# Optimization experiments

Hardware: AMD Instinct MI355X
Metric: run time of the kernel (lower is better)

## Reference

```python
import jax, jax.numpy as jnp
import numpy as np

INPUT_DIM = 16
LW = 128          # layerwidth
NB_LAYERS = 4
NB_X = 4096
NB_THETA = 128
PARAM_COUNT = INPUT_DIM * LW + LW + (NB_LAYERS - 1) * (LW * LW + LW) + LW + 1  # 51841


def setup_inputs() -> dict:
    k1, k2 = jax.random.split(jax.random.key(0))
    x = jax.random.normal(k1, (NB_X, INPUT_DIM), dtype=jnp.float32)
    theta = jax.random.normal(k2, (NB_THETA, PARAM_COUNT), dtype=jnp.float32)
    return {"x": x, "theta": theta}


def reference(x, theta):
    # x: [nb_x, input_dim], theta: [nb_theta, param_count]
    t = theta.shape[0]
    off = 0
    # first layer: W0 [t, LW, INPUT_DIM], b0 [t, LW]
    W0 = theta[:, off:off + INPUT_DIM * LW].reshape(t, LW, INPUT_DIM); off += INPUT_DIM * LW
    b0 = theta[:, off:off + LW]; off += LW
    h = jnp.tanh(jnp.einsum('thi,xi->txh', W0, x) + b0[:, None, :])  # [t, nb_x, LW]
    # hidden layers
    for _ in range(NB_LAYERS - 1):
        W = theta[:, off:off + LW * LW].reshape(t, LW, LW); off += LW * LW
        b = theta[:, off:off + LW]; off += LW
        h = jnp.tanh(jnp.einsum('tho,txo->txh', W, h) + b[:, None, :])
    # output layer: Wl [t, LW], bl [t, 1]
    Wl = theta[:, off:off + LW]; off += LW
    bl = theta[:, off:off + 1]
    out = jnp.einsum('th,txh->tx', Wl, h)[..., None] + bl[:, None, :]  # [t, nb_x, 1]
    return out
```

## Files before the change

### kernel.cpp

```cpp
#include <hip/hip_runtime.h>


#define IND      16
#define LWD      128
#define THREADS  256
#define PARAMS   51841

#define HID_STRIDE 36864
#define WS_W0    (128 * 3 * HID_STRIDE)
#define WS_XI    (WS_W0 + 128 * 16384)
#define WS_TOTAL (WS_XI + 32 * 8192)

#define LDS_WL   36864
#define LDS_BL   37376
#define LDS_SZ   37380

typedef _Float16 f16x8 __attribute__((ext_vector_type(8)));
typedef _Float16 f16x4 __attribute__((ext_vector_type(4)));
typedef float    f32x16 __attribute__((ext_vector_type(16)));
typedef unsigned u32x2  __attribute__((ext_vector_type(2)));

union U4 { unsigned u[4]; f16x8 v; };

__device__ __forceinline__ f32x16 zero16() {
    f32x16 z;
#pragma unroll
    for (int i = 0; i < 16; ++i) z[i] = 0.0f;
    return z;
}
__device__ __forceinline__ float fast_tanh(float v) {
    float e = __builtin_amdgcn_exp2f(v * 2.8853900817779268f);
    return 1.0f - 2.0f * __builtin_amdgcn_rcpf(e + 1.0f);
}
__device__ __forceinline__ unsigned pkf16(float a, float b) {
    unsigned short ua = __builtin_bit_cast(unsigned short, (_Float16)a);
    unsigned short ub = __builtin_bit_cast(unsigned short, (_Float16)b);
    return (unsigned)ua | ((unsigned)ub << 16);
}
#define MFMA(A, B, C) __builtin_amdgcn_mfma_f32_32x32x16_f16((A), (B), (C), 0, 0, 0)

__device__ __forceinline__ void gload16(const void* g, void* l) {
    __builtin_amdgcn_global_load_lds(
        (const __attribute__((address_space(1))) void*)g,
        (__attribute__((address_space(3))) void*)l, 16, 0, 0);
}

__device__ __forceinline__ void conv8(const float* __restrict__ s, char* hidst, char* lodst) {
    float v[8];
    *reinterpret_cast<float4*>(v)     = *reinterpret_cast<const float4*>(s);
    *reinterpret_cast<float4*>(v + 4) = *reinterpret_cast<const float4*>(s + 4);
    f16x8 hi, lo;
#pragma unroll
    for (int i = 0; i < 8; ++i) {
        hi[i] = (_Float16)v[i];
        lo[i] = (_Float16)(v[i] - (float)hi[i]);
    }
    *reinterpret_cast<f16x8*>(hidst) = hi;
    *reinterpret_cast<f16x8*>(lodst) = lo;
}

__global__ __launch_bounds__(256)
void prep_kernel(const float* __restrict__ theta, const float* __restrict__ xin,
                 char* __restrict__ ws)
{
    const int b = blockIdx.x, tid = threadIdx.x;
    if (b < 3072) {
        const int t = b / 24, rem = b % 24, li = rem >> 3, hblk = rem & 7;
        const int h  = hblk * 16 + (tid >> 4);
        const int kc = (tid >> 1) & 7, kh = tid & 1;
        const float* src = theta + (size_t)t * PARAMS + 2176 + li * 16512
                         + h * 128 + kc * 16 + kh * 8;
        float v[8];
        *reinterpret_cast<float4*>(v)     = *reinterpret_cast<const float4*>(src);
        *reinterpret_cast<float4*>(v + 4) = *reinterpret_cast<const float4*>(src + 4);
        f16x8 p;
#pragma unroll
        for (int i = 0; i < 8; ++i) p[i] = (_Float16)v[i];
        char* img = ws + (size_t)(t * 3 + li) * HID_STRIDE;
        *reinterpret_cast<f16x8*>(img + ((h >> 5) * 9 + kc) * 1024
                                      + (kh * 32 + (h & 31)) * 16) = p;
    } else if (b < 3456) {
        const int idx = b - 3072, t = idx / 3, li = idx % 3;
        const int tt = tid >> 6, l6 = tid & 63, kh = l6 >> 5, row = l6 & 31;
        f16x8 p;
#pragma unroll
        for (int i = 0; i < 8; ++i) p[i] = (_Float16)0.0f;
        if (kh == 0) {
            const float bv = theta[(size_t)t * PARAMS + 2176 + li * 16512
                                   + 16384 + tt * 32 + row];
            p[0] = (_Float16)bv;
            p[1] = (_Float16)(bv - (float)p[0]);
        }
        char* img = ws + (size_t)(t * 3 + li) * HID_STRIDE;
        *reinterpret_cast<f16x8*>(img + (tt * 9 + 8) * 1024 + l6 * 16) = p;
    } else if (b < 3520) {
        const int gid = (b - 3456) * 256 + tid;
        const int t = gid >> 7, h = gid & 127;
        const float* src = theta + (size_t)t * PARAMS + h * IND;
        char* dst = ws + WS_W0 + (size_t)t * 16384 + h * 32;
        conv8(src,     dst,      dst + 4096);
        conv8(src + 8, dst + 16, dst + 4096 + 16);
    } else if (b < 3648) {
        const int t = b - 3520;
        const float* th = theta + (size_t)t * PARAMS;
        char* base = ws + WS_W0 + (size_t)t * 16384;
        {
            const int tt = tid >> 6, l6 = tid & 63, kh = l6 >> 5, row = l6 & 31;
            f16x8 p;
#pragma unroll
            for (int i = 0; i < 8; ++i) p[i] = (_Float16)0.0f;
            if (kh == 0) {
                const float bv = th[2048 + tt * 32 + row];
                p[0] = (_Float16)bv;
                p[1] = (_Float16)(bv - (float)p[0]);
            }
            *reinterpret_cast<f16x8*>(base + 8192 + tt * 1024 + l6 * 16) = p;
        }
        if (tid < 32) {
            const int kc = tid >> 1, kh = tid & 1;
            const float* src = th + 51712 + kc * 16 + kh * 8;
            f16x8 p;
#pragma unroll
            for (int i = 0; i < 8; ++i) p[i] = (_Float16)src[i];
            *reinterpret_cast<f16x8*>(base + 12288 + tid * 16) = p;
        }
    } else {
        const int row = (b - 3648) * 256 + tid;
        const float* src = xin + (size_t)row * IND;
        char* dst = ws + WS_XI + (size_t)(row >> 7) * 8192 + (row & 127) * 32;
        conv8(src,     dst,      dst + 4096);
        conv8(src + 8, dst + 16, dst + 4096 + 16);
    }
}

__global__ __launch_bounds__(THREADS, 4)
void mlp_main(const float* __restrict__ theta, const char* __restrict__ ws,
              float* __restrict__ out)
{
    __shared__ __align__(16) char sL[LDS_SZ];

    const int tid = threadIdx.x, bid = blockIdx.x;
    const int sw  = (bid & 7) * 512 + (bid >> 3);
    const int t   = sw >> 5, xt = sw & 31;
    const float* __restrict__ th = theta + (size_t)t * PARAMS;
    const int lane = tid & 63, w = tid >> 6, r31 = lane & 31, khalf = lane >> 5;
    const int bpa  = (lane ^ 32) << 2;
    (void)bpa;

    U4 ubias;
    ubias.u[0] = khalf ? 0u : 0x3C003C00u;
    ubias.u[1] = 0u; ubias.u[2] = 0u; ubias.u[3] = 0u;
    const f16x8 Bones = ubias.v;

    {
        const char* img = ws + (size_t)(t * 3) * HID_STRIDE;
#pragma unroll
        for (int c = 0; c < 9; ++c)
            gload16(img + (c * 4 + w) * 1024 + lane * 16, sL + (c * 4 + w) * 1024);
        if (tid < 32)
            gload16(ws + WS_W0 + (size_t)t * 16384 + 12288 + tid * 16,
                    sL + LDS_WL + tid * 16);
        if (tid == 32) *reinterpret_cast<float*>(sL + LDS_BL) = th[51840];
    }

    f32x16 acc[4];
    {
        const char* w0i = ws + WS_W0 + (size_t)t  * 16384;
        const char* xi  = ws + WS_XI + (size_t)xt * 8192;
        const int ro = r31 * 32 + khalf * 16;
        const f16x8 B0h = *reinterpret_cast<const f16x8*>(xi + w * 1024 + ro);
        const f16x8 B0l = *reinterpret_cast<const f16x8*>(xi + 4096 + w * 1024 + ro);
#pragma unroll
        for (int tt = 0; tt < 4; ++tt) {
            f32x16 a = zero16();
            const f16x8 Ab = *reinterpret_cast<const f16x8*>(w0i + 8192 + tt * 1024 + lane * 16);
            a = MFMA(Ab, Bones, a);
            const f16x8 Ah = *reinterpret_cast<const f16x8*>(w0i + tt * 1024 + ro);
            const f16x8 Al = *reinterpret_cast<const f16x8*>(w0i + 4096 + tt * 1024 + ro);
            a = MFMA(Al, B0h, a);
            a = MFMA(Ah, B0l, a);
            a = MFMA(Ah, B0h, a);
            acc[tt] = a;
        }
    }

    f16x8 Bf[8];
    auto activate_pack = [&]() {
#pragma unroll
        for (int tt = 0; tt < 4; ++tt) {
            unsigned P0[4], P1[4];
#pragma unroll
            for (int g = 0; g < 4; ++g) {
                const float v0 = fast_tanh(acc[tt][4 * g + 0]);
                const float v1 = fast_tanh(acc[tt][4 * g + 1]);
                const float v2 = fast_tanh(acc[tt][4 * g + 2]);
                const float v3 = fast_tanh(acc[tt][4 * g + 3]);
                P0[g] = pkf16(v0, v1);
                P1[g] = pkf16(v2, v3);
            }
#pragma unroll
            for (int j = 0; j < 2; ++j) {
#if __has_builtin(__builtin_amdgcn_permlane32_swap)
                const u32x2 r0 = __builtin_amdgcn_permlane32_swap(
                    P0[2 * j], P0[2 * j + 1], false, false);
                const u32x2 r1 = __builtin_amdgcn_permlane32_swap(
                    P1[2 * j], P1[2 * j + 1], false, false);
                U4 u;
                u.u[0] = r0[0]; u.u[1] = r1[0]; u.u[2] = r0[1]; u.u[3] = r1[1];
#else
                const unsigned s0 = khalf ? P0[2 * j] : P0[2 * j + 1];
                const unsigned s1 = khalf ? P1[2 * j] : P1[2 * j + 1];
                const unsigned q0 = (unsigned)__builtin_amdgcn_ds_bpermute(bpa, (int)s0);
                const unsigned q1 = (unsigned)__builtin_amdgcn_ds_bpermute(bpa, (int)s1);
                U4 u;
                u.u[0] = khalf ? q0 : P0[2 * j];
                u.u[1] = khalf ? q1 : P1[2 * j];
                u.u[2] = khalf ? P0[2 * j + 1] : q0;
                u.u[3] = khalf ? P1[2 * j + 1] : q1;
#endif
                Bf[2 * tt + j] = u.v;
            }
        }
    };
    activate_pack();
    __syncthreads();

#pragma unroll
    for (int l = 1; l <= 3; ++l) {
        __builtin_amdgcn_s_setprio(1);
#pragma unroll
        for (int tt = 0; tt < 4; ++tt) {
            f32x16 a = zero16();
            a = MFMA(*reinterpret_cast<const f16x8*>(
                         sL + (tt * 9 + 8) * 1024 + lane * 16), Bones, a);
#pragma unroll
            for (int kc = 0; kc < 8; ++kc) {
                const f16x8 av = *reinterpret_cast<const f16x8*>(
                    sL + (tt * 9 + kc) * 1024 + lane * 16);
                a = MFMA(av, Bf[kc], a);
            }
            acc[tt] = a;
        }
        __builtin_amdgcn_s_setprio(0);
        if (l < 3) {
            __syncthreads();
            const char* img = ws + (size_t)(t * 3 + l) * HID_STRIDE;
#pragma unroll
            for (int c = 0; c < 9; ++c)
                gload16(img + (c * 4 + w) * 1024 + lane * 16, sL + (c * 4 + w) * 1024);
            activate_pack();
            __syncthreads();
        }
    }

    activate_pack();
    const float bl = *reinterpret_cast<const float*>(sL + LDS_BL);
    f32x16 af = zero16();
#pragma unroll
    for (int kc = 0; kc < 8; ++kc) {
        const f16x8 wv = *reinterpret_cast<const f16x8*>(
            sL + LDS_WL + (kc * 2 + khalf) * 16);
        af = MFMA(wv, Bf[kc], af);
    }
    if (!khalf) out[(size_t)t * 4096 + xt * 128 + w * 32 + r31] = af[0] + bl;
}

__global__ __launch_bounds__(THREADS, 1)
void mlp_kernel_fb(const float* __restrict__ xin,
                   const float* __restrict__ theta,
                   float* __restrict__ out)
{
    __shared__ __align__(16) _Float16 sH   [128 * LWD];
    __shared__ __align__(16) _Float16 sWhi [LWD * LWD];
    __shared__ __align__(16) _Float16 sWlo [LWD * LWD];
    __shared__ __align__(16) _Float16 sX0hi[128 * IND];
    __shared__ __align__(16) _Float16 sX0lo[128 * IND];
    __shared__ __align__(16) _Float16 sW0hi[LWD * IND];
    __shared__ __align__(16) _Float16 sW0lo[LWD * IND];
    __shared__ float sB[2][LWD];
    __shared__ float sWl[LWD + 1];

    const int tid = threadIdx.x;
    const int bid = blockIdx.x;
    const int sw  = (bid & 7) * 512 + (bid >> 3);
    const int t   = sw >> 5;
    const int xt  = sw & 31;
    const float* __restrict__ th = theta + (size_t)t * PARAMS;
    const float* __restrict__ xg = xin   + (size_t)xt * (128 * IND);

#pragma unroll
    for (int j = 0; j < 2; ++j) {
        const int flat = j * 1024 + tid * 4;
        const float4 v = *reinterpret_cast<const float4*>(xg + flat);
        _Float16 h0 = (_Float16)v.x, h1 = (_Float16)v.y, h2 = (_Float16)v.z, h3 = (_Float16)v.w;
        f16x4 ph = {h0, h1, h2, h3};
        f16x4 pl = {(_Float16)(v.x - (float)h0), (_Float16)(v.y - (float)h1),
                    (_Float16)(v.z - (float)h2), (_Float16)(v.w - (float)h3)};
        *reinterpret_cast<f16x4*>(&sX0hi[flat]) = ph;
        *reinterpret_cast<f16x4*>(&sX0lo[flat]) = pl;
    }
#pragma unroll
    for (int j = 0; j < 2; ++j) {
        const int flat = j * 1024 + tid * 4;
        const float a0 = th[flat], a1 = th[flat + 1], a2 = th[flat + 2], a3 = th[flat + 3];
        _Float16 h0 = (_Float16)a0, h1 = (_Float16)a1, h2 = (_Float16)a2, h3 = (_Float16)a3;
        f16x4 ph = {h0, h1, h2, h3};
        f16x4 pl = {(_Float16)(a0 - (float)h0), (_Float16)(a1 - (float)h1),
                    (_Float16)(a2 - (float)h2), (_Float16)(a3 - (float)h3)};
        *reinterpret_cast<f16x4*>(&sW0hi[flat]) = ph;
        *reinterpret_cast<f16x4*>(&sW0lo[flat]) = pl;
    }
    if (tid < LWD) sB[0][tid] = th[IND * LWD + tid];
    __syncthreads();

    const int lane  = tid & 63;
    const int w     = tid >> 6;
    const int r31   = lane & 31;
    const int khalf = lane >> 5;
    const int hb    = (w >> 1) * 64;
    const int xb    = (w & 1) * 64;
    const int hA0 = hb + r31,  hA1 = hb + 32 + r31;
    const int xB0 = xb + r31,  xB1 = xb + 32 + r31;
    const int swzA0 = (hA0 & 15) << 4, swzA1 = (hA1 & 15) << 4;
    const int swzB0 = (xB0 & 15) << 4, swzB1 = (xB1 & 15) << 4;

    f32x16 acc[2][2];

    {
        const int kb = khalf * 16;
        f16x8 ah[2], al[2], bh[2], bl[2];
        ah[0] = *reinterpret_cast<const f16x8*>((const char*)sW0hi + hA0 * 32 + kb);
        ah[1] = *reinterpret_cast<const f16x8*>((const char*)sW0hi + hA1 * 32 + kb);
        al[0] = *reinterpret_cast<const f16x8*>((const char*)sW0lo + hA0 * 32 + kb);
        al[1] = *reinterpret_cast<const f16x8*>((const char*)sW0lo + hA1 * 32 + kb);
        bh[0] = *reinterpret_cast<const f16x8*>((const char*)sX0hi + xB0 * 32 + kb);
        bh[1] = *reinterpret_cast<const f16x8*>((const char*)sX0hi + xB1 * 32 + kb);
        bl[0] = *reinterpret_cast<const f16x8*>((const char*)sX0lo + xB0 * 32 + kb);
        bl[1] = *reinterpret_cast<const f16x8*>((const char*)sX0lo + xB1 * 32 + kb);
#pragma unroll
        for (int tt = 0; tt < 2; ++tt)
#pragma unroll
            for (int tx = 0; tx < 2; ++tx) {
                f32x16 a;
#pragma unroll
                for (int i = 0; i < 16; ++i) a[i] = 0.0f;
                a = MFMA(al[tt], bh[tx], a);
                a = MFMA(ah[tt], bl[tx], a);
                a = MFMA(ah[tt], bh[tx], a);
                acc[tt][tx] = a;
            }
    }

    auto epilogue = [&](const float* __restrict__ bb) {
#pragma unroll
        for (int tt = 0; tt < 2; ++tt)
#pragma unroll
            for (int tx = 0; tx < 2; ++tx) {
                const int xw  = xb + tx * 32 + r31;
                const int swz = (xw & 15) << 4;
#pragma unroll
                for (int g = 0; g < 4; ++g) {
                    const int hbase = hb + tt * 32 + g * 8 + khalf * 4;
                    f16x4 pk;
#pragma unroll
                    for (int q = 0; q < 4; ++q) {
                        const float v = acc[tt][tx][g * 4 + q] + bb[hbase + q];
                        pk[q] = (_Float16)(1.0f - 2.0f * __builtin_amdgcn_rcpf(
                            __builtin_amdgcn_exp2f(v * 2.8853900817779268f) + 1.0f));
                    }
                    *reinterpret_cast<f16x4*>((char*)sH + xw * 256 + ((hbase * 2) ^ swz)) = pk;
                }
            }
    };

    for (int l = 0; l < 3; ++l) {
        __syncthreads();
        const float* __restrict__ wsrc = th + 2176 + l * 16512;
#pragma unroll
        for (int j = 0; j < 16; ++j) {
            const int flat = j * 1024 + tid * 4;
            const int hrow = flat >> 7;
            const int o    = flat & 127;
            const float a0 = wsrc[flat], a1 = wsrc[flat + 1], a2 = wsrc[flat + 2], a3 = wsrc[flat + 3];
            _Float16 h0 = (_Float16)a0, h1 = (_Float16)a1, h2 = (_Float16)a2, h3 = (_Float16)a3;
            f16x4 ph = {h0, h1, h2, h3};
            f16x4 pl = {(_Float16)(a0 - (float)h0), (_Float16)(a1 - (float)h1),
                        (_Float16)(a2 - (float)h2), (_Float16)(a3 - (float)h3)};
            const int boff = hrow * 256 + ((o * 2) ^ ((hrow & 15) << 4));
            *reinterpret_cast<f16x4*>((char*)sWhi + boff) = ph;
            *reinterpret_cast<f16x4*>((char*)sWlo + boff) = pl;
        }
        if (tid < LWD) sB[(l + 1) & 1][tid] = wsrc[LWD * LWD + tid];
        if (l == 2) {
            if (tid < LWD) sWl[tid] = th[51712 + tid];
            if (tid == LWD) sWl[LWD] = th[51840];
        }

        epilogue(sB[l & 1]);
        __syncthreads();

#pragma unroll
        for (int tt = 0; tt < 2; ++tt)
#pragma unroll
            for (int tx = 0; tx < 2; ++tx)
#pragma unroll
                for (int i = 0; i < 16; ++i) acc[tt][tx][i] = 0.0f;
#pragma unroll
        for (int kc = 0; kc < 8; ++kc) {
            const int kb = kc * 32 + khalf * 16;
            f16x8 ah[2], al[2], bv[2];
            ah[0] = *reinterpret_cast<const f16x8*>((const char*)sWhi + hA0 * 256 + (kb ^ swzA0));
            ah[1] = *reinterpret_cast<const f16x8*>((const char*)sWhi + hA1 * 256 + (kb ^ swzA1));
            al[0] = *reinterpret_cast<const f16x8*>((const char*)sWlo + hA0 * 256 + (kb ^ swzA0));
            al[1] = *reinterpret_cast<const f16x8*>((const char*)sWlo + hA1 * 256 + (kb ^ swzA1));
            bv[0] = *reinterpret_cast<const f16x8*>((const char*)sH   + xB0 * 256 + (kb ^ swzB0));
            bv[1] = *reinterpret_cast<const f16x8*>((const char*)sH   + xB1 * 256 + (kb ^ swzB1));
#pragma unroll
            for (int tt = 0; tt < 2; ++tt)
#pragma unroll
                for (int tx = 0; tx < 2; ++tx) {
                    acc[tt][tx] = MFMA(al[tt], bv[tx], acc[tt][tx]);
                    acc[tt][tx] = MFMA(ah[tt], bv[tx], acc[tt][tx]);
                }
        }
    }

    __syncthreads();
    epilogue(sB[1]);
    __syncthreads();

    if (tid < 128) {
        const int r   = tid;
        const int swz = (r & 15) << 4;
        float s = 0.0f;
#pragma unroll
        for (int c = 0; c < 16; ++c) {
            const int hc = (c + r) & 15;
            const f16x8 hv = *reinterpret_cast<const f16x8*>(
                (const char*)sH + r * 256 + ((hc * 16) ^ swz));
#pragma unroll
            for (int q = 0; q < 8; ++q) s += (float)hv[q] * sWl[hc * 8 + q];
        }
        out[(size_t)t * 4096 + (size_t)xt * 128 + r] = s + sWl[LWD];
    }
}

extern "C" void kernel_launch(void* const* d_in, const int* in_sizes, int n_in,
                              void* d_out, int out_size, void* d_ws, size_t ws_size,
                              hipStream_t stream)
{
    const float* x     = (const float*)d_in[0];
    const float* theta = (const float*)d_in[1];
    float* out = (float*)d_out;

    if (ws_size >= (size_t)WS_TOTAL) {
        prep_kernel<<<dim3(3664), dim3(256), 0, stream>>>(theta, x, (char*)d_ws);
        mlp_main<<<dim3(4096), dim3(THREADS), 0, stream>>>(theta, (const char*)d_ws, out);
    } else {
        mlp_kernel_fb<<<dim3(4096), dim3(THREADS), 0, stream>>>(x, theta, out);
    }
}
```

Baseline: 109.6 us.

## Interleave tanh packing with MFMA chunks and fold tanh scale into weights

Restructures each hidden layer so the tanh-and-pack of one output tile is interleaved with the MFMA k-chunks that consume already-packed tiles, using double-buffered accumulators. This lets VALU transcendental work overlap the matrix pipeline instead of running as a separate phase. It also pre-multiplies weights and biases by 2/ln2 in the prep kernel, so the activation skips one multiply. The activation itself becomes a sign-symmetric form with a polynomial-plus-Newton reciprocal and a packed round-toward-zero convert. The occupancy hint drops from 4 to 2 blocks per CU, which allows more registers but may cut latency hiding. The weight scaling and the different reciprocal and rounding slightly change numerics.

Measured after the change: 118.4 us. +8.0%, slower.

```diff
diff --git a/kernel.cpp b/kernel.cpp
--- a/kernel.cpp
+++ b/kernel.cpp
@@ -5,6 +5,7 @@
 #define LWD      128
 #define THREADS  256
 #define PARAMS   51841
+#define SCALE    2.8853900817779268f
 
 #define HID_STRIDE 36864
 #define WS_W0    (128 * 3 * HID_STRIDE)
@@ -28,15 +29,22 @@
     for (int i = 0; i < 16; ++i) z[i] = 0.0f;
     return z;
 }
-__device__ __forceinline__ float fast_tanh(float v) {
-    float e = __builtin_amdgcn_exp2f(v * 2.8853900817779268f);
-    return 1.0f - 2.0f * __builtin_amdgcn_rcpf(e + 1.0f);
-}
-__device__ __forceinline__ unsigned pkf16(float a, float b) {
-    unsigned short ua = __builtin_bit_cast(unsigned short, (_Float16)a);
-    unsigned short ub = __builtin_bit_cast(unsigned short, (_Float16)b);
-    return (unsigned)ua | ((unsigned)ub << 16);
-}
+
+__device__ __forceinline__ unsigned tanh2pk(float z0, float z1) {
+    const float t0 = __builtin_amdgcn_exp2f(-__builtin_fabsf(z0));
+    const float t1 = __builtin_amdgcn_exp2f(-__builtin_fabsf(z1));
+    const float d0 = t0 + 1.0f, d1 = t1 + 1.0f;
+    float r0 = __builtin_fmaf(d0, __builtin_fmaf(d0, 0.32302f, -1.45380f), 2.12094f);
+    float r1 = __builtin_fmaf(d1, __builtin_fmaf(d1, 0.32302f, -1.45380f), 2.12094f);
+    r0 = __builtin_fmaf(r0, __builtin_fmaf(-d0, r0, 1.0f), r0);
+    r1 = __builtin_fmaf(r1, __builtin_fmaf(-d1, r1, 1.0f), r1);
+    const float u0 = __builtin_fmaf(t0 * r0, -2.0f, 1.0f);
+    const float u1 = __builtin_fmaf(t1 * r1, -2.0f, 1.0f);
+    const float y0 = __builtin_copysignf(u0, z0);
+    const float y1 = __builtin_copysignf(u1, z1);
+    return __builtin_bit_cast(unsigned, __builtin_amdgcn_cvt_pkrtz(y0, y1));
+}
+
 #define MFMA(A, B, C) __builtin_amdgcn_mfma_f32_32x32x16_f16((A), (B), (C), 0, 0, 0)
 
 __device__ __forceinline__ void gload16(const void* g, void* l) {
@@ -45,15 +53,17 @@
         (__attribute__((address_space(3))) void*)l, 16, 0, 0);
 }
 
-__device__ __forceinline__ void conv8(const float* __restrict__ s, char* hidst, char* lodst) {
+__device__ __forceinline__ void conv8(const float* __restrict__ s, char* hidst,
+                                      char* lodst, float scale) {
     float v[8];
     *reinterpret_cast<float4*>(v)     = *reinterpret_cast<const float4*>(s);
     *reinterpret_cast<float4*>(v + 4) = *reinterpret_cast<const float4*>(s + 4);
     f16x8 hi, lo;
 #pragma unroll
     for (int i = 0; i < 8; ++i) {
-        hi[i] = (_Float16)v[i];
-        lo[i] = (_Float16)(v[i] - (float)hi[i]);
+        const float sv = v[i] * scale;
+        hi[i] = (_Float16)sv;
+        lo[i] = (_Float16)(sv - (float)hi[i]);
     }
     *reinterpret_cast<f16x8*>(hidst) = hi;
     *reinterpret_cast<f16x8*>(lodst) = lo;
@@ -75,7 +85,7 @@
         *reinterpret_cast<float4*>(v + 4) = *reinterpret_cast<const float4*>(src + 4);
         f16x8 p;
 #pragma unroll
-        for (int i = 0; i < 8; ++i) p[i] = (_Float16)v[i];
+        for (int i = 0; i < 8; ++i) p[i] = (_Float16)(v[i] * SCALE);
         char* img = ws + (size_t)(t * 3 + li) * HID_STRIDE;
         *reinterpret_cast<f16x8*>(img + ((h >> 5) * 9 + kc) * 1024
                                       + (kh * 32 + (h & 31)) * 16) = p;
@@ -86,8 +96,8 @@
 #pragma unroll
         for (int i = 0; i < 8; ++i) p[i] = (_Float16)0.0f;
         if (kh == 0) {
-            const float bv = theta[(size_t)t * PARAMS + 2176 + li * 16512
-                                   + 16384 + tt * 32 + row];
+            const float bv = SCALE * theta[(size_t)t * PARAMS + 2176 + li * 16512
+                                           + 16384 + tt * 32 + row];
             p[0] = (_Float16)bv;
             p[1] = (_Float16)(bv - (float)p[0]);
         }
@@ -98,8 +108,8 @@
         const int t = gid >> 7, h = gid & 127;
         const float* src = theta + (size_t)t * PARAMS + h * IND;
         char* dst = ws + WS_W0 + (size_t)t * 16384 + h * 32;
-        conv8(src,     dst,      dst + 4096);
-        conv8(src + 8, dst + 16, dst + 4096 + 16);
+        conv8(src,     dst,      dst + 4096,      SCALE);
+        conv8(src + 8, dst + 16, dst + 4096 + 16, SCALE);
     } else if (b < 3648) {
         const int t = b - 3520;
         const float* th = theta + (size_t)t * PARAMS;
@@ -110,7 +120,7 @@
 #pragma unroll
             for (int i = 0; i < 8; ++i) p[i] = (_Float16)0.0f;
             if (kh == 0) {
-                const float bv = th[2048 + tt * 32 + row];
+                const float bv = SCALE * th[2048 + tt * 32 + row];
                 p[0] = (_Float16)bv;
                 p[1] = (_Float16)(bv - (float)p[0]);
             }
@@ -128,12 +138,12 @@
         const int row = (b - 3648) * 256 + tid;
         const float* src = xin + (size_t)row * IND;
         char* dst = ws + WS_XI + (size_t)(row >> 7) * 8192 + (row & 127) * 32;
-        conv8(src,     dst,      dst + 4096);
-        conv8(src + 8, dst + 16, dst + 4096 + 16);
-    }
-}
-
-__global__ __launch_bounds__(THREADS, 4)
+        conv8(src,     dst,      dst + 4096,      1.0f);
+        conv8(src + 8, dst + 16, dst + 4096 + 16, 1.0f);
+    }
+}
+
+__global__ __launch_bounds__(THREADS, 2)
 void mlp_main(const float* __restrict__ theta, const char* __restrict__ ws,
               float* __restrict__ out)
 {
@@ -151,19 +161,24 @@
     ubias.u[0] = khalf ? 0u : 0x3C003C00u;
     ubias.u[1] = 0u; ubias.u[2] = 0u; ubias.u[3] = 0u;
     const f16x8 Bones = ubias.v;
-
-    {
-        const char* img = ws + (size_t)(t * 3) * HID_STRIDE;
+    const f32x16 Z = zero16();
+
+    auto stage = [&](int l) {
+        const char* img = ws + (size_t)(t * 3 + l) * HID_STRIDE;
 #pragma unroll
         for (int c = 0; c < 9; ++c)
             gload16(img + (c * 4 + w) * 1024 + lane * 16, sL + (c * 4 + w) * 1024);
-        if (tid < 32)
-            gload16(ws + WS_W0 + (size_t)t * 16384 + 12288 + tid * 16,
-                    sL + LDS_WL + tid * 16);
-        if (tid == 32) *reinterpret_cast<float*>(sL + LDS_BL) = th[51840];
-    }
-
-    f32x16 acc[4];
+    };
+
+    stage(0);
+    if (tid < 32)
+        gload16(ws + WS_W0 + (size_t)t * 16384 + 12288 + tid * 16,
+                sL + LDS_WL + tid * 16);
+    if (tid == 32) *reinterpret_cast<float*>(sL + LDS_BL) = th[51840];
+
+    f32x16 accA[4], accB[4];
+    f16x8  Bf[8];
+
     {
         const char* w0i = ws + WS_W0 + (size_t)t  * 16384;
         const char* xi  = ws + WS_XI + (size_t)xt * 8192;
@@ -172,96 +187,99 @@
         const f16x8 B0l = *reinterpret_cast<const f16x8*>(xi + 4096 + w * 1024 + ro);
 #pragma unroll
         for (int tt = 0; tt < 4; ++tt) {
-            f32x16 a = zero16();
             const f16x8 Ab = *reinterpret_cast<const f16x8*>(w0i + 8192 + tt * 1024 + lane * 16);
-            a = MFMA(Ab, Bones, a);
+            f32x16 a = MFMA(Ab, Bones, Z);
             const f16x8 Ah = *reinterpret_cast<const f16x8*>(w0i + tt * 1024 + ro);
             const f16x8 Al = *reinterpret_cast<const f16x8*>(w0i + 4096 + tt * 1024 + ro);
             a = MFMA(Al, B0h, a);
             a = MFMA(Ah, B0l, a);
             a = MFMA(Ah, B0h, a);
-            acc[tt] = a;
-        }
-    }
-
-    f16x8 Bf[8];
-    auto activate_pack = [&]() {
+            accA[tt] = a;
+        }
+    }
+
+    auto pack_tile = [&](const f32x16& a, int bi) {
+        unsigned P0[4], P1[4];
+#pragma unroll
+        for (int g = 0; g < 4; ++g) {
+            P0[g] = tanh2pk(a[4 * g + 0], a[4 * g + 1]);
+            P1[g] = tanh2pk(a[4 * g + 2], a[4 * g + 3]);
+        }
+#pragma unroll
+        for (int j = 0; j < 2; ++j) {
+#if __has_builtin(__builtin_amdgcn_permlane32_swap)
+            const u32x2 r0 = __builtin_amdgcn_permlane32_swap(
+                P0[2 * j], P0[2 * j + 1], false, false);
+            const u32x2 r1 = __builtin_amdgcn_permlane32_swap(
+                P1[2 * j], P1[2 * j + 1], false, false);
+            U4 u;
+            u.u[0] = r0[0]; u.u[1] = r1[0]; u.u[2] = r0[1]; u.u[3] = r1[1];
+#else
+            const unsigned s0 = khalf ? P0[2 * j] : P0[2 * j + 1];
+            const unsigned s1 = khalf ? P1[2 * j] : P1[2 * j + 1];
+            const unsigned q0 = (unsigned)__builtin_amdgcn_ds_bpermute(bpa, (int)s0);
+            const unsigned q1 = (unsigned)__builtin_amdgcn_ds_bpermute(bpa, (int)s1);
+            U4 u;
+            u.u[0] = khalf ? q0 : P0[2 * j];
+            u.u[1] = khalf ? q1 : P1[2 * j];
+            u.u[2] = khalf ? P0[2 * j + 1] : q0;
+            u.u[3] = khalf ? P1[2 * j + 1] : q1;
+#endif
+            Bf[bi + j] = u.v;
+        }
+    };
+
+    auto kchunk = [&](f32x16* aN, int kc) {
 #pragma unroll
         for (int tt = 0; tt < 4; ++tt) {
-            unsigned P0[4], P1[4];
-#pragma unroll
-            for (int g = 0; g < 4; ++g) {
-                const float v0 = fast_tanh(acc[tt][4 * g + 0]);
-                const float v1 = fast_tanh(acc[tt][4 * g + 1]);
-                const float v2 = fast_tanh(acc[tt][4 * g + 2]);
-                const float v3 = fast_tanh(acc[tt][4 * g + 3]);
-                P0[g] = pkf16(v0, v1);
-                P1[g] = pkf16(v2, v3);
-            }
-#pragma unroll
-            for (int j = 0; j < 2; ++j) {
-#if __has_builtin(__builtin_amdgcn_permlane32_swap)
-                const u32x2 r0 = __builtin_amdgcn_permlane32_swap(
-                    P0[2 * j], P0[2 * j + 1], false, false);
-                const u32x2 r1 = __builtin_amdgcn_permlane32_swap(
-                    P1[2 * j], P1[2 * j + 1], false, false);
-                U4 u;
-                u.u[0] = r0[0]; u.u[1] = r1[0]; u.u[2] = r0[1]; u.u[3] = r1[1];
-#else
-                const unsigned s0 = khalf ? P0[2 * j] : P0[2 * j + 1];
-                const unsigned s1 = khalf ? P1[2 * j] : P1[2 * j + 1];
-                const unsigned q0 = (unsigned)__builtin_amdgcn_ds_bpermute(bpa, (int)s0);
-                const unsigned q1 = (unsigned)__builtin_amdgcn_ds_bpermute(bpa, (int)s1);
-                U4 u;
-                u.u[0] = khalf ? q0 : P0[2 * j];
-                u.u[1] = khalf ? q1 : P1[2 * j];
-                u.u[2] = khalf ? P0[2 * j + 1] : q0;
-                u.u[3] = khalf ? P1[2 * j + 1] : q1;
-#endif
-                Bf[2 * tt + j] = u.v;
-            }
+            const f16x8 av = *reinterpret_cast<const f16x8*>(
+                sL + (tt * 9 + kc) * 1024 + lane * 16);
+            aN[tt] = MFMA(av, Bf[kc], aN[tt]);
         }
     };
-    activate_pack();
-    __syncthreads();
-
-#pragma unroll
-    for (int l = 1; l <= 3; ++l) {
-        __builtin_amdgcn_s_setprio(1);
-#pragma unroll
-        for (int tt = 0; tt < 4; ++tt) {
-            f32x16 a = zero16();
-            a = MFMA(*reinterpret_cast<const f16x8*>(
-                         sL + (tt * 9 + 8) * 1024 + lane * 16), Bones, a);
-#pragma unroll
-            for (int kc = 0; kc < 8; ++kc) {
-                const f16x8 av = *reinterpret_cast<const f16x8*>(
-                    sL + (tt * 9 + kc) * 1024 + lane * 16);
-                a = MFMA(av, Bf[kc], a);
-            }
-            acc[tt] = a;
-        }
-        __builtin_amdgcn_s_setprio(0);
-        if (l < 3) {
-            __syncthreads();
-            const char* img = ws + (size_t)(t * 3 + l) * HID_STRIDE;
-#pragma unroll
-            for (int c = 0; c < 9; ++c)
-                gload16(img + (c * 4 + w) * 1024 + lane * 16, sL + (c * 4 + w) * 1024);
-            activate_pack();
-            __syncthreads();
-        }
-    }
-
-    activate_pack();
+
+    auto body = [&](const f32x16* aO, f32x16* aN) {
+#pragma unroll
+        for (int tt = 0; tt < 4; ++tt)
+            aN[tt] = MFMA(*reinterpret_cast<const f16x8*>(
+                              sL + (tt * 9 + 8) * 1024 + lane * 16), Bones, Z);
+        pack_tile(aO[1], 2);
+        kchunk(aN, 0); kchunk(aN, 1);
+        pack_tile(aO[2], 4);
+        kchunk(aN, 2); kchunk(aN, 3);
+        pack_tile(aO[3], 6);
+        kchunk(aN, 4); kchunk(aN, 5); kchunk(aN, 6); kchunk(aN, 7);
+    };
+
+    pack_tile(accA[0], 0);
+    __syncthreads();
+    body(accA, accB);
+
+    __syncthreads();
+    stage(1);
+    pack_tile(accB[0], 0);
+    __syncthreads();
+    body(accB, accA);
+
+    __syncthreads();
+    stage(2);
+    pack_tile(accA[0], 0);
+    __syncthreads();
+    body(accA, accB);
+
     const float bl = *reinterpret_cast<const float*>(sL + LDS_BL);
-    f32x16 af = zero16();
-#pragma unroll
-    for (int kc = 0; kc < 8; ++kc) {
-        const f16x8 wv = *reinterpret_cast<const f16x8*>(
-            sL + LDS_WL + (kc * 2 + khalf) * 16);
-        af = MFMA(wv, Bf[kc], af);
-    }
+    pack_tile(accB[0], 0);
+    pack_tile(accB[1], 2);
+    f32x16 af = MFMA(*reinterpret_cast<const f16x8*>(sL + LDS_WL + (khalf) * 16), Bf[0], Z);
+    af = MFMA(*reinterpret_cast<const f16x8*>(sL + LDS_WL + (2 + khalf) * 16), Bf[1], af);
+    pack_tile(accB[2], 4);
+    af = MFMA(*reinterpret_cast<const f16x8*>(sL + LDS_WL + (4 + khalf) * 16), Bf[2], af);
+    af = MFMA(*reinterpret_cast<const f16x8*>(sL + LDS_WL + (6 + khalf) * 16), Bf[3], af);
+    pack_tile(accB[3], 6);
+    af = MFMA(*reinterpret_cast<const f16x8*>(sL + LDS_WL + (8 + khalf) * 16), Bf[4], af);
+    af = MFMA(*reinterpret_cast<const f16x8*>(sL + LDS_WL + (10 + khalf) * 16), Bf[5], af);
+    af = MFMA(*reinterpret_cast<const f16x8*>(sL + LDS_WL + (12 + khalf) * 16), Bf[6], af);
+    af = MFMA(*reinterpret_cast<const f16x8*>(sL + LDS_WL + (14 + khalf) * 16), Bf[7], af);
     if (!khalf) out[(size_t)t * 4096 + xt * 128 + w * 32 + r31] = af[0] + bl;
 }
 
```
